# Kernel tuning notes

Measured on AMD Instinct MI355X. Metric: run time of the kernel, lower is better.

The kernel has to match this reference:

```python
import jax, jax.numpy as jnp
import numpy as np
from jax import lax

B, L, H = 2, 1024, 1024
D = 2048          # intermediate_size
N = 16            # ssm state size
K = 4             # conv kernel
R = 64            # time_step_rank


def setup_inputs() -> dict:
    key = jax.random.key(0)
    ks = jax.random.split(key, 10)
    def nrm(k, shape, scale=0.02):
        return jax.random.normal(k, shape, dtype=jnp.float32) * scale
    A = jnp.arange(1, N + 1, dtype=jnp.float32)[None, :] * jnp.ones((D, 1), jnp.float32)
    return {
        "hidden_states": jax.random.normal(ks[0], (B, L, H), dtype=jnp.float32),
        "W_in":  nrm(ks[1], (2 * D, H)),
        "conv_w": nrm(ks[2], (D, 1, K), 0.1),
        "conv_b": nrm(ks[3], (D,), 0.1),
        "W_x":   nrm(ks[4], (R + 2 * N, D)),
        "W_dt":  nrm(ks[5], (D, R), 0.1),
        "b_dt":  jnp.full((D,), -4.6, jnp.float32),  # softplus(-4.6) ~ 0.01 dt init
        "A_log": jnp.log(A),
        "D_param": jnp.ones((D,), jnp.float32),
        "W_out": nrm(ks[6], (H, D)),
    }


def _mamba_forward(hidden_states, W_in, conv_w, conv_b, W_x, W_dt, b_dt, A_log, D_param, W_out):
    silu = jax.nn.silu
    # in_proj -> [B, L, 2D], chunk into x and gate
    proj = jnp.einsum("blh,eh->ble", hidden_states, W_in)
    x, gate = jnp.split(proj, 2, axis=-1)           # [B,L,D] each
    # depthwise causal conv over time: [B,D,L]
    xc = x.swapaxes(1, 2)
    xc = lax.conv_general_dilated(
        xc, conv_w, window_strides=(1,), padding=[(K - 1, 0)],
        dimension_numbers=("NCH", "OIH", "NCH"), feature_group_count=D)
    x = silu(xc + conv_b[None, :, None]).swapaxes(1, 2)   # [B,L,D]
    # x_proj -> dt, Bmat, Cmat
    ssm_p = jnp.einsum("bld,rd->blr", x, W_x)             # [B,L,R+2N]
    dt_lr, Bm, Cm = ssm_p[..., :R], ssm_p[..., R:R + N], ssm_p[..., R + N:]
    dt = jax.nn.softplus(jnp.einsum("blr,dr->bld", dt_lr, W_dt) + b_dt)  # [B,L,D]
    A = -jnp.exp(A_log)                                   # [D,N]
    dA = jnp.exp(dt[..., None] * A[None, None])           # [B,L,D,N]
    dBu = dt[..., None] * Bm[:, :, None, :] * x[..., None]  # [B,L,D,N]
    # selective scan over time
    def step(h, inp):
        dA_t, dBu_t, C_t = inp                            # [B,D,N],[B,D,N],[B,N]
        h = dA_t * h + dBu_t
        y = jnp.einsum("bdn,bn->bd", h, C_t)
        return h, y
    h0 = jnp.zeros((B, D, N), dt.dtype)
    _, ys = lax.scan(step, h0, (dA.swapaxes(0, 1), dBu.swapaxes(0, 1), Cm.swapaxes(0, 1)))
    y = ys.swapaxes(0, 1)                                 # [B,L,D]
    y = (y + x * D_param[None, None, :]) * silu(gate)
    return jnp.einsum("bld,hd->blh", y, W_out)            # [B,L,H]


def reference(hidden_states, W_in, conv_w, conv_b, W_x, W_dt, b_dt, A_log, D_param, W_out):
    return _mamba_forward(hidden_states, W_in, conv_w, conv_b, W_x, W_dt, b_dt, A_log, D_param, W_out)
```

## Files before the change

### kernel.cpp

```cpp
#include <hip/hip_runtime.h>
#include <hip/hip_bf16.h>
#include <math.h>

#define B_ 2
#define L_ 1024
#define H_ 1024
#define D_ 2048
#define N_ 16
#define R_ 64
#define NCK 32
#define CL 32

typedef short short8 __attribute__((ext_vector_type(8)));
typedef float floatx4 __attribute__((ext_vector_type(4)));

__device__ __forceinline__ float siluf(float g) {
    return g / (1.0f + __expf(-g));
}

__device__ __forceinline__ unsigned short f2bf(float f) {
    unsigned int u = __float_as_uint(f);
    u = (u + 0x7fffu + ((u >> 16) & 1u)) >> 16;
    return (unsigned short)u;
}

__device__ __forceinline__ float bf2f(unsigned short u) {
    return __uint_as_float(((unsigned int)u) << 16);
}

__device__ __forceinline__ void gl2lds(const unsigned short* g, unsigned short* l) {
    __builtin_amdgcn_global_load_lds(
        (const __attribute__((address_space(1))) unsigned int*)g,
        (__attribute__((address_space(3))) unsigned int*)l, 16, 0, 0);
}

#define Q0 524288
#define Q1 1572864
#define Q2 2097152
#define Q3 2146304
#define Q4 2179072
__global__ __launch_bounds__(256) void cvt_all(
    const float* __restrict__ i0, const float* __restrict__ i1,
    const float* __restrict__ i2, const float* __restrict__ i3,
    const float* __restrict__ i4,
    unsigned short* __restrict__ o0, unsigned short* __restrict__ o1,
    unsigned short* __restrict__ o2, unsigned short* __restrict__ o3,
    unsigned short* __restrict__ o4)
{
    int q = blockIdx.x * 256 + threadIdx.x;
    if (q >= Q4) return;
    const float* in; unsigned short* out; int base;
    if (q < Q0)      { in = i0; out = o0; base = 0; }
    else if (q < Q1) { in = i1; out = o1; base = Q0; }
    else if (q < Q2) { in = i2; out = o2; base = Q1; }
    else if (q < Q3) { in = i3; out = o3; base = Q2; }
    else             { in = i4; out = o4; base = Q3; }
    int i = (q - base) * 4;
    float4 v = *(const float4*)(in + i);
    ushort4 o;
    o.x = f2bf(v.x); o.y = f2bf(v.y); o.z = f2bf(v.z); o.w = f2bf(v.w);
    *(ushort4*)(out + i) = o;
}

template<int EPI>
__global__ __launch_bounds__(256) void gemm_bf16_nt(
    const unsigned short* __restrict__ A, const unsigned short* __restrict__ Bm,
    float* __restrict__ C, int K, int Ncols, int ldc, int kChunk, int nMax,
    size_t partStride, float* __restrict__ C2)
{
    __shared__ unsigned short As[128 * 32];
    __shared__ unsigned short Bs[128 * 32];
    const int tid  = threadIdx.x;
    const int lane = tid & 63;
    const int wave = tid >> 6;
    const int wm = (wave >> 1) * 64;
    const int wn = (wave & 1) * 64;
    const int lr   = lane & 15;
    const int quad = lane >> 4;
    const int m0 = blockIdx.y * 128;
    const int n0 = blockIdx.x * 128;
    const int k0 = blockIdx.z * kChunk;

    const int srow = wave * 32 + (lane >> 2);
    const int sq   = (lane & 3) * 8;
    unsigned short* AsB0 = &As[(wave * 32) * 32];
    unsigned short* AsB1 = &As[(wave * 32 + 16) * 32];
    unsigned short* BsB0 = &Bs[(wave * 32) * 32];
    unsigned short* BsB1 = &Bs[(wave * 32 + 16) * 32];
    const size_t aoff0 = (size_t)(m0 + srow) * K + sq;
    const size_t aoff1 = (size_t)(m0 + srow + 16) * K + sq;
    const size_t boff0 = (size_t)min(n0 + srow, nMax - 1) * K + sq;
    const size_t boff1 = (size_t)min(n0 + srow + 16, nMax - 1) * K + sq;

    floatx4 acc[4][4];
#pragma unroll
    for (int mi = 0; mi < 4; ++mi)
#pragma unroll
        for (int ni = 0; ni < 4; ++ni)
            acc[mi][ni] = (floatx4){0.f, 0.f, 0.f, 0.f};

    for (int kt = k0; kt < k0 + kChunk; kt += 32) {
        __syncthreads();
        gl2lds(A + aoff0 + kt, AsB0);
        gl2lds(A + aoff1 + kt, AsB1);
        gl2lds(Bm + boff0 + kt, BsB0);
        gl2lds(Bm + boff1 + kt, BsB1);
        __syncthreads();
        short8 af[4], bf[4];
#pragma unroll
        for (int mi = 0; mi < 4; ++mi)
            af[mi] = *(const short8*)&As[(wm + mi * 16 + lr) * 32 + quad * 8];
#pragma unroll
        for (int ni = 0; ni < 4; ++ni)
            bf[ni] = *(const short8*)&Bs[(wn + ni * 16 + lr) * 32 + quad * 8];
#pragma unroll
        for (int mi = 0; mi < 4; ++mi)
#pragma unroll
            for (int ni = 0; ni < 4; ++ni)
                acc[mi][ni] = __builtin_amdgcn_mfma_f32_16x16x32_bf16(
                    af[mi], bf[ni], acc[mi][ni], 0, 0, 0);
    }

    float* Cz = C + (size_t)blockIdx.z * partStride;
#pragma unroll
    for (int mi = 0; mi < 4; ++mi)
#pragma unroll
        for (int ni = 0; ni < 4; ++ni) {
            const int rr = m0 + wm + mi * 16 + quad * 4;
            const int cc = n0 + wn + ni * 16 + lr;
            if (cc >= Ncols) continue;
            if (EPI == 4) {
                if (n0 < 2048) {
                    float4 v = make_float4(acc[mi][ni][0], acc[mi][ni][1],
                                           acc[mi][ni][2], acc[mi][ni][3]);
                    *(float4*)&C[(size_t)cc * ldc + rr] = v;
                } else {
#pragma unroll
                    for (int r = 0; r < 4; ++r)
                        C2[(size_t)(rr + r) * 2048 + (cc - 2048)] = acc[mi][ni][r];
                }
            } else {
#pragma unroll
                for (int r = 0; r < 4; ++r)
                    Cz[(size_t)(rr + r) * ldc + cc] = acc[mi][ni][r];
            }
        }
}

__global__ __launch_bounds__(256) void reduce_ssm(
    const float* __restrict__ P, float* __restrict__ ssm_p,
    unsigned short* __restrict__ sp64)
{
    const int q = blockIdx.x * 256 + threadIdx.x;
    const int m = q / 24;
    const int c = (q - m * 24) * 4;
    const size_t idx = (size_t)m * 96 + c;
    float4 s = make_float4(0.f, 0.f, 0.f, 0.f);
#pragma unroll
    for (int z = 0; z < 16; ++z) {
        float4 v = *(const float4*)(P + (size_t)z * (2048 * 96) + idx);
        s.x += v.x; s.y += v.y; s.z += v.z; s.w += v.w;
    }
    *(float4*)(ssm_p + idx) = s;
    if (c < 64) {
        ushort4 o;
        o.x = f2bf(s.x); o.y = f2bf(s.y); o.z = f2bf(s.z); o.w = f2bf(s.w);
        *(ushort4*)(sp64 + (size_t)m * 64 + c) = o;
    }
}

__global__ __launch_bounds__(256) void reduce_out(
    const float* __restrict__ P, float* __restrict__ out)
{
    const size_t i = ((size_t)blockIdx.x * 256 + threadIdx.x) * 4;
    float4 a = *(const float4*)(P + i);
    float4 b = *(const float4*)(P + 2097152 + i);
    float4 c = *(const float4*)(P + 2 * 2097152 + i);
    float4 d = *(const float4*)(P + 3 * 2097152 + i);
    *(float4*)(out + i) = make_float4(a.x + b.x + c.x + d.x,
                                      a.y + b.y + c.y + d.y,
                                      a.z + b.z + c.z + d.z,
                                      a.w + b.w + c.w + d.w);
}

__global__ __launch_bounds__(256) void dt_gemm(
    const unsigned short* __restrict__ A,
    const unsigned short* __restrict__ Bm,
    float* __restrict__ C,
    const float* __restrict__ bias)
{
    __shared__ unsigned short As[64 * 72];
    __shared__ unsigned short Bs[64 * 72];
    const int tid = threadIdx.x;
    const int lane = tid & 63;
    const int wave = tid >> 6;
    const int lr = lane & 15;
    const int quad = lane >> 4;
    const int n0 = blockIdx.x * 64;
    const int m0 = blockIdx.y * 64;

    {
        const int row = tid >> 3;
        const int cq = (tid & 7) * 8;
        uint4 a0 = *(const uint4*)(A + (size_t)(m0 + row) * 64 + cq);
        uint4 a1 = *(const uint4*)(A + (size_t)(m0 + 32 + row) * 64 + cq);
        uint4 b0 = *(const uint4*)(Bm + (size_t)(n0 + row) * 64 + cq);
        uint4 b1 = *(const uint4*)(Bm + (size_t)(n0 + 32 + row) * 64 + cq);
        *(uint4*)&As[row * 72 + cq] = a0;
        *(uint4*)&As[(32 + row) * 72 + cq] = a1;
        *(uint4*)&Bs[row * 72 + cq] = b0;
        *(uint4*)&Bs[(32 + row) * 72 + cq] = b1;
    }
    __syncthreads();

    floatx4 acc[4];
#pragma unroll
    for (int ni = 0; ni < 4; ++ni) acc[ni] = (floatx4){0.f, 0.f, 0.f, 0.f};

#pragma unroll
    for (int kt = 0; kt < 64; kt += 32) {
        short8 af = *(const short8*)&As[(wave * 16 + lr) * 72 + kt + quad * 8];
#pragma unroll
        for (int ni = 0; ni < 4; ++ni) {
            short8 bf = *(const short8*)&Bs[(ni * 16 + lr) * 72 + kt + quad * 8];
            acc[ni] = __builtin_amdgcn_mfma_f32_16x16x32_bf16(af, bf, acc[ni], 0, 0, 0);
        }
    }

    const int rr = m0 + wave * 16 + quad * 4;
#pragma unroll
    for (int ni = 0; ni < 4; ++ni) {
        const int cc = n0 + ni * 16 + lr;
        const float bv = bias[cc];
#pragma unroll
        for (int r = 0; r < 4; ++r) {
            const float z = acc[ni][r] + bv;
            const float spv = fmaxf(z, 0.f) + __logf(1.f + __expf(-fabsf(z)));
            C[(size_t)(rr + r) * 2048 + cc] = spv;
        }
    }
}

__global__ __launch_bounds__(256) void conv_silu_kernel(
    const float* __restrict__ projx, const float* __restrict__ conv_w,
    const float* __restrict__ conv_b, unsigned short* __restrict__ x_bf)
{
    __shared__ unsigned short tile[64][72];
    const int t = threadIdx.x;
    const int d0 = blockIdx.x * 64;
    const int lt0 = blockIdx.y * 64;
    const int b = blockIdx.z;
    const int dl = t & 63;
    const int seg = t >> 6;
    const int d = d0 + dl;
    const int l0 = lt0 + seg * 16;
    const float* row = projx + (size_t)d * 2048 + b * 1024;
    const float w0 = conv_w[d * 4 + 0], w1 = conv_w[d * 4 + 1];
    const float w2 = conv_w[d * 4 + 2], w3 = conv_w[d * 4 + 3];
    const float bias = conv_b[d];

    float p[19];
    p[0] = (l0 >= 3) ? row[l0 - 3] : 0.f;
    p[1] = (l0 >= 2) ? row[l0 - 2] : 0.f;
    p[2] = (l0 >= 1) ? row[l0 - 1] : 0.f;
#pragma unroll
    for (int j = 0; j < 16; j += 4) {
        float4 q = *(const float4*)(row + l0 + j);
        p[3 + j] = q.x; p[4 + j] = q.y; p[5 + j] = q.z; p[6 + j] = q.w;
    }
#pragma unroll
    for (int j = 0; j < 16; ++j) {
        float v = siluf(bias + w0 * p[j] + w1 * p[j + 1] + w2 * p[j + 2] + w3 * p[j + 3]);
        tile[seg * 16 + j][dl] = f2bf(v);
    }
    __syncthreads();

    const int ml = t >> 2;
    const int c = t & 3;
    short8 s0 = *(const short8*)&tile[ml][c * 16];
    short8 s1 = *(const short8*)&tile[ml][c * 16 + 8];
    unsigned short* dst = x_bf + (size_t)(b * 1024 + lt0 + ml) * 2048 + d0 + c * 16;
    *(short8*)dst = s0;
    *(short8*)(dst + 8) = s1;
}

__global__ __launch_bounds__(256) void scan_p1(
    const float* __restrict__ dt, const unsigned short* __restrict__ x_bf,
    const float* __restrict__ sp, const float* __restrict__ A_log,
    float* __restrict__ Pch, float* __restrict__ Hch)
{
    __shared__ float sB[CL][16];
    const int tid = threadIdx.x;
    const int d = blockIdx.x * 256 + tid;
    const int ck = blockIdx.y;
    const int b = blockIdx.z;
    const int mb = b * 1024 + ck * CL;

    if (tid < CL * 4) {
        int row = tid >> 2, q = (tid & 3) * 4;
        *(float4*)&sB[row][q] = *(const float4*)(sp + (size_t)(mb + row) * 96 + 64 + q);
    }
    float An2[16];
    {
        const float* al = A_log + d * 16;
#pragma unroll
        for (int j = 0; j < 16; j += 4) {
            float4 a4 = *(const float4*)(al + j);
            An2[j + 0] = -__expf(a4.x) * 1.44269504f;
            An2[j + 1] = -__expf(a4.y) * 1.44269504f;
            An2[j + 2] = -__expf(a4.z) * 1.44269504f;
            An2[j + 3] = -__expf(a4.w) * 1.44269504f;
        }
    }
    __syncthreads();

    float h[16];
#pragma unroll
    for (int n = 0; n < 16; ++n) h[n] = 0.f;
    float dts = 0.f;

    for (int l = 0; l < CL; ++l) {
        const size_t off = (size_t)(mb + l) * 2048 + d;
        const float dtv = dt[off];
        const float xv = bf2f(x_bf[off]);
        const float u = dtv * xv;
        dts += dtv;
        float4 B0 = *(const float4*)&sB[l][0];
        float4 B1 = *(const float4*)&sB[l][4];
        float4 B2 = *(const float4*)&sB[l][8];
        float4 B3 = *(const float4*)&sB[l][12];
        float Bv[16] = {B0.x, B0.y, B0.z, B0.w, B1.x, B1.y, B1.z, B1.w,
                        B2.x, B2.y, B2.z, B2.w, B3.x, B3.y, B3.z, B3.w};
#pragma unroll
        for (int n = 0; n < 16; ++n) {
            const float dA = __builtin_amdgcn_exp2f(dtv * An2[n]);
            h[n] = fmaf(dA, h[n], Bv[n] * u);
        }
    }

    const size_t base = ((size_t)(b * NCK + ck) * 2048 + d) * 16;
#pragma unroll
    for (int j = 0; j < 16; j += 4) {
        float4 pv = make_float4(__builtin_amdgcn_exp2f(dts * An2[j]),
                                __builtin_amdgcn_exp2f(dts * An2[j + 1]),
                                __builtin_amdgcn_exp2f(dts * An2[j + 2]),
                                __builtin_amdgcn_exp2f(dts * An2[j + 3]));
        *(float4*)(Pch + base + j) = pv;
        *(float4*)(Hch + base + j) = make_float4(h[j], h[j + 1], h[j + 2], h[j + 3]);
    }
}

__global__ __launch_bounds__(256) void scan_combine(
    float* __restrict__ Pch, const float* __restrict__ Hch)
{
    const int flat = blockIdx.x * 256 + threadIdx.x;
    const int dn = flat & 32767;
    const int b = flat >> 15;
    float hin = 0.f;
#pragma unroll 4
    for (int ck = 0; ck < NCK; ++ck) {
        const size_t a = ((size_t)(b * NCK + ck) << 15) + dn;
        const float p = Pch[a];
        const float hc = Hch[a];
        Pch[a] = hin;
        hin = fmaf(p, hin, hc);
    }
}

__global__ __launch_bounds__(256) void scan_p2(
    const float* __restrict__ dt, const unsigned short* __restrict__ x_bf,
    const float* __restrict__ gate, const float* __restrict__ sp,
    const float* __restrict__ A_log, const float* __restrict__ Dp,
    const float* __restrict__ Hin, unsigned short* __restrict__ y_bf)
{
    __shared__ float sBC[CL][32];
    const int tid = threadIdx.x;
    const int d = blockIdx.x * 256 + tid;
    const int ck = blockIdx.y;
    const int b = blockIdx.z;
    const int mb = b * 1024 + ck * CL;

    {
        int row = tid >> 3, q = (tid & 7) * 4;
        *(float4*)&sBC[row][q] = *(const float4*)(sp + (size_t)(mb + row) * 96 + 64 + q);
    }
    float An2[16];
    {
        const float* al = A_log + d * 16;
#pragma unroll
        for (int j = 0; j < 16; j += 4) {
            float4 a4 = *(const float4*)(al + j);
            An2[j + 0] = -__expf(a4.x) * 1.44269504f;
            An2[j + 1] = -__expf(a4.y) * 1.44269504f;
            An2[j + 2] = -__expf(a4.z) * 1.44269504f;
            An2[j + 3] = -__expf(a4.w) * 1.44269504f;
        }
    }
    float h[16];
    {
        const size_t base = ((size_t)(b * NCK + ck) * 2048 + d) * 16;
#pragma unroll
        for (int j = 0; j < 16; j += 4) {
            float4 hv = *(const float4*)(Hin + base + j);
            h[j] = hv.x; h[j + 1] = hv.y; h[j + 2] = hv.z; h[j + 3] = hv.w;
        }
    }
    const float Dv = Dp[d];
    __syncthreads();

    for (int l = 0; l < CL; ++l) {
        const size_t off = (size_t)(mb + l) * 2048 + d;
        const float dtv = dt[off];
        const float xv = bf2f(x_bf[off]);
        const float gv = gate[off];
        const float u = dtv * xv;
        float4 B0 = *(const float4*)&sBC[l][0];
        float4 B1 = *(const float4*)&sBC[l][4];
        float4 B2 = *(const float4*)&sBC[l][8];
        float4 B3 = *(const float4*)&sBC[l][12];
        float Bv[16] = {B0.x, B0.y, B0.z, B0.w, B1.x, B1.y, B1.z, B1.w,
                        B2.x, B2.y, B2.z, B2.w, B3.x, B3.y, B3.z, B3.w};
#pragma unroll
        for (int n = 0; n < 16; ++n) {
            const float dA = __builtin_amdgcn_exp2f(dtv * An2[n]);
            h[n] = fmaf(dA, h[n], Bv[n] * u);
        }
        float4 C0 = *(const float4*)&sBC[l][16];
        float4 C1 = *(const float4*)&sBC[l][20];
        float4 C2 = *(const float4*)&sBC[l][24];
        float4 C3 = *(const float4*)&sBC[l][28];
        float Cv[16] = {C0.x, C0.y, C0.z, C0.w, C1.x, C1.y, C1.z, C1.w,
                        C2.x, C2.y, C2.z, C2.w, C3.x, C3.y, C3.z, C3.w};
        float p = 0.f;
#pragma unroll
        for (int n = 0; n < 16; ++n)
            p = fmaf(h[n], Cv[n], p);
        y_bf[off] = f2bf(fmaf(xv, Dv, p) * siluf(gv));
    }
}

extern "C" void kernel_launch(void* const* d_in, const int* in_sizes, int n_in,
                              void* d_out, int out_size, void* d_ws, size_t ws_size,
                              hipStream_t stream)
{
    const float* hs     = (const float*)d_in[0];
    const float* W_in   = (const float*)d_in[1];
    const float* conv_w = (const float*)d_in[2];
    const float* conv_b = (const float*)d_in[3];
    const float* W_x    = (const float*)d_in[4];
    const float* W_dt   = (const float*)d_in[5];
    const float* b_dt   = (const float*)d_in[6];
    const float* A_log  = (const float*)d_in[7];
    const float* Dp     = (const float*)d_in[8];
    const float* W_out  = (const float*)d_in[9];
    float* out = (float*)d_out;

    float* ws    = (float*)d_ws;
    float* gate  = ws;
    float* dtb   = gate + (size_t)4194304;
    float* projx = dtb + (size_t)4194304;
    float* ssm_p = projx + (size_t)4194304;
    unsigned short* hs_bf    = (unsigned short*)(ssm_p + 196608);
    unsigned short* W_in_bf  = hs_bf + (size_t)2097152;
    unsigned short* W_out_bf = W_in_bf + (size_t)4194304;
    unsigned short* W_x_bf   = W_out_bf + (size_t)2097152;
    unsigned short* W_dt_bf  = W_x_bf + (size_t)196608;
    unsigned short* sp64_bf  = W_dt_bf + (size_t)131072;
    unsigned short* x_bf     = sp64_bf + (size_t)131072;
    float* P1   = projx;
    float* Pch  = projx;
    float* Hch  = projx + (size_t)2097152;
    float* Pout = gate;
    unsigned short* y_bf = hs_bf;

    const int M = B_ * L_;

    cvt_all<<<(Q4 + 255) / 256, 256, 0, stream>>>(
        hs, W_in, W_out, W_x, W_dt, hs_bf, W_in_bf, W_out_bf, W_x_bf, W_dt_bf);

    gemm_bf16_nt<4><<<dim3(4096 / 128, M / 128, 1), 256, 0, stream>>>(
        hs_bf, W_in_bf, projx, 1024, 4096, 2048, 1024, 4096, 0, gate);

    conv_silu_kernel<<<dim3(D_ / 64, L_ / 64, B_), 256, 0, stream>>>(
        projx, conv_w, conv_b, x_bf);

    gemm_bf16_nt<0><<<dim3(1, M / 128, 16), 256, 0, stream>>>(
        x_bf, W_x_bf, P1, 2048, 96, 96, 128, 96, (size_t)2048 * 96, nullptr);

    reduce_ssm<<<(2048 * 24) / 256, 256, 0, stream>>>(P1, ssm_p, sp64_bf);

    dt_gemm<<<dim3(2048 / 64, 2048 / 64), 256, 0, stream>>>(
        sp64_bf, W_dt_bf, dtb, b_dt);

    scan_p1<<<dim3(D_ / 256, NCK, B_), 256, 0, stream>>>(
        dtb, x_bf, ssm_p, A_log, Pch, Hch);
    scan_combine<<<(B_ * D_ * 16) / 256, 256, 0, stream>>>(Pch, Hch);
    scan_p2<<<dim3(D_ / 256, NCK, B_), 256, 0, stream>>>(
        dtb, x_bf, gate, ssm_p, A_log, Dp, Pch, y_bf);

    gemm_bf16_nt<0><<<dim3(1024 / 128, M / 128, 4), 256, 0, stream>>>(
        y_bf, W_out_bf, Pout, 2048, 1024, 1024, 512, 1024, (size_t)2048 * 1024, nullptr);

    reduce_out<<<(2048 * 1024 / 4) / 256, 256, 0, stream>>>(Pout, out);
}
```

Baseline: 237.0 us.

## Store projected x and dt intermediates in bf16 with LDS-staged transposed epilogue

The in_proj GEMM now writes the transposed x half as bf16, staging the tile through shared memory so each row is written with coalesced 16-byte stores. The conv kernel reads this bf16 buffer, and dt_gemm writes softplus(dt) as bf16, which both scan passes then read. This halves the memory traffic for two large [B,L,D] intermediates. The cost is reduced precision on x before the conv and on dt, which feeds the exponentials in the scan, plus extra syncthreads in the GEMM epilogue.

```diff
diff --git a/kernel.cpp b/kernel.cpp
--- a/kernel.cpp
+++ b/kernel.cpp
@@ -121,30 +121,67 @@
                     af[mi], bf[ni], acc[mi][ni], 0, 0, 0);
     }
 
-    float* Cz = C + (size_t)blockIdx.z * partStride;
-#pragma unroll
-    for (int mi = 0; mi < 4; ++mi)
-#pragma unroll
-        for (int ni = 0; ni < 4; ++ni) {
-            const int rr = m0 + wm + mi * 16 + quad * 4;
-            const int cc = n0 + wn + ni * 16 + lr;
-            if (cc >= Ncols) continue;
-            if (EPI == 4) {
-                if (n0 < 2048) {
-                    float4 v = make_float4(acc[mi][ni][0], acc[mi][ni][1],
-                                           acc[mi][ni][2], acc[mi][ni][3]);
-                    *(float4*)&C[(size_t)cc * ldc + rr] = v;
-                } else {
+    if constexpr (EPI == 4) {
+        if (n0 < 2048) {
+            __shared__ unsigned short Ct[64 * 136];
+            unsigned short* Cb = (unsigned short*)C;
+#pragma unroll
+            for (int h = 0; h < 2; ++h) {
+                __syncthreads();
+                if ((wave & 1) == h) {
+#pragma unroll
+                    for (int mi = 0; mi < 4; ++mi)
+#pragma unroll
+                        for (int ni = 0; ni < 4; ++ni) {
+                            const int ccl = ni * 16 + lr;
+                            const int rrl = wm + mi * 16 + quad * 4;
+                            ushort4 v;
+                            v.x = f2bf(acc[mi][ni][0]);
+                            v.y = f2bf(acc[mi][ni][1]);
+                            v.z = f2bf(acc[mi][ni][2]);
+                            v.w = f2bf(acc[mi][ni][3]);
+                            *(ushort4*)&Ct[ccl * 136 + rrl] = v;
+                        }
+                }
+                __syncthreads();
+                const int row = tid >> 2;
+                const int mq = (tid & 3) * 32;
+                uint4 w0 = *(const uint4*)&Ct[row * 136 + mq];
+                uint4 w1 = *(const uint4*)&Ct[row * 136 + mq + 8];
+                uint4 w2 = *(const uint4*)&Ct[row * 136 + mq + 16];
+                uint4 w3 = *(const uint4*)&Ct[row * 136 + mq + 24];
+                unsigned short* dst = Cb + (size_t)(n0 + h * 64 + row) * 2048 + m0 + mq;
+                *(uint4*)dst = w0;
+                *(uint4*)(dst + 8) = w1;
+                *(uint4*)(dst + 16) = w2;
+                *(uint4*)(dst + 24) = w3;
+            }
+        } else {
+#pragma unroll
+            for (int mi = 0; mi < 4; ++mi)
+#pragma unroll
+                for (int ni = 0; ni < 4; ++ni) {
+                    const int rr = m0 + wm + mi * 16 + quad * 4;
+                    const int cc = n0 + wn + ni * 16 + lr - 2048;
 #pragma unroll
                     for (int r = 0; r < 4; ++r)
-                        C2[(size_t)(rr + r) * 2048 + (cc - 2048)] = acc[mi][ni][r];
+                        C2[(size_t)(rr + r) * 2048 + cc] = acc[mi][ni][r];
                 }
-            } else {
+        }
+    } else {
+        float* Cz = C + (size_t)blockIdx.z * partStride;
+#pragma unroll
+        for (int mi = 0; mi < 4; ++mi)
+#pragma unroll
+            for (int ni = 0; ni < 4; ++ni) {
+                const int rr = m0 + wm + mi * 16 + quad * 4;
+                const int cc = n0 + wn + ni * 16 + lr;
+                if (cc >= Ncols) continue;
 #pragma unroll
                 for (int r = 0; r < 4; ++r)
                     Cz[(size_t)(rr + r) * ldc + cc] = acc[mi][ni][r];
             }
-        }
+    }
 }
 
 __global__ __launch_bounds__(256) void reduce_ssm(
@@ -186,7 +223,7 @@
 __global__ __launch_bounds__(256) void dt_gemm(
     const unsigned short* __restrict__ A,
     const unsigned short* __restrict__ Bm,
-    float* __restrict__ C,
+    unsigned short* __restrict__ C,
     const float* __restrict__ bias)
 {
     __shared__ unsigned short As[64 * 72];
@@ -236,13 +273,13 @@
         for (int r = 0; r < 4; ++r) {
             const float z = acc[ni][r] + bv;
             const float spv = fmaxf(z, 0.f) + __logf(1.f + __expf(-fabsf(z)));
-            C[(size_t)(rr + r) * 2048 + cc] = spv;
+            C[(size_t)(rr + r) * 2048 + cc] = f2bf(spv);
         }
     }
 }
 
 __global__ __launch_bounds__(256) void conv_silu_kernel(
-    const float* __restrict__ projx, const float* __restrict__ conv_w,
+    const unsigned short* __restrict__ projx, const float* __restrict__ conv_w,
     const float* __restrict__ conv_b, unsigned short* __restrict__ x_bf)
 {
     __shared__ unsigned short tile[64][72];
@@ -254,19 +291,23 @@
     const int seg = t >> 6;
     const int d = d0 + dl;
     const int l0 = lt0 + seg * 16;
-    const float* row = projx + (size_t)d * 2048 + b * 1024;
+    const unsigned short* row = projx + (size_t)d * 2048 + b * 1024;
     const float w0 = conv_w[d * 4 + 0], w1 = conv_w[d * 4 + 1];
     const float w2 = conv_w[d * 4 + 2], w3 = conv_w[d * 4 + 3];
     const float bias = conv_b[d];
 
     float p[19];
-    p[0] = (l0 >= 3) ? row[l0 - 3] : 0.f;
-    p[1] = (l0 >= 2) ? row[l0 - 2] : 0.f;
-    p[2] = (l0 >= 1) ? row[l0 - 1] : 0.f;
-#pragma unroll
-    for (int j = 0; j < 16; j += 4) {
-        float4 q = *(const float4*)(row + l0 + j);
-        p[3 + j] = q.x; p[4 + j] = q.y; p[5 + j] = q.z; p[6 + j] = q.w;
+    p[0] = (l0 >= 3) ? bf2f(row[l0 - 3]) : 0.f;
+    p[1] = (l0 >= 2) ? bf2f(row[l0 - 2]) : 0.f;
+    p[2] = (l0 >= 1) ? bf2f(row[l0 - 1]) : 0.f;
+    {
+        short8 q0 = *(const short8*)(row + l0);
+        short8 q1 = *(const short8*)(row + l0 + 8);
+#pragma unroll
+        for (int j = 0; j < 8; ++j) {
+            p[3 + j] = bf2f((unsigned short)q0[j]);
+            p[11 + j] = bf2f((unsigned short)q1[j]);
+        }
     }
 #pragma unroll
     for (int j = 0; j < 16; ++j) {
@@ -285,7 +326,7 @@
 }
 
 __global__ __launch_bounds__(256) void scan_p1(
-    const float* __restrict__ dt, const unsigned short* __restrict__ x_bf,
+    const unsigned short* __restrict__ dt, const unsigned short* __restrict__ x_bf,
     const float* __restrict__ sp, const float* __restrict__ A_log,
     float* __restrict__ Pch, float* __restrict__ Hch)
 {
@@ -321,7 +362,7 @@
 
     for (int l = 0; l < CL; ++l) {
         const size_t off = (size_t)(mb + l) * 2048 + d;
-        const float dtv = dt[off];
+        const float dtv = bf2f(dt[off]);
         const float xv = bf2f(x_bf[off]);
         const float u = dtv * xv;
         dts += dtv;
@@ -368,7 +409,7 @@
 }
 
 __global__ __launch_bounds__(256) void scan_p2(
-    const float* __restrict__ dt, const unsigned short* __restrict__ x_bf,
+    const unsigned short* __restrict__ dt, const unsigned short* __restrict__ x_bf,
     const float* __restrict__ gate, const float* __restrict__ sp,
     const float* __restrict__ A_log, const float* __restrict__ Dp,
     const float* __restrict__ Hin, unsigned short* __restrict__ y_bf)
@@ -410,7 +451,7 @@
 
     for (int l = 0; l < CL; ++l) {
         const size_t off = (size_t)(mb + l) * 2048 + d;
-        const float dtv = dt[off];
+        const float dtv = bf2f(dt[off]);
         const float xv = bf2f(x_bf[off]);
         const float gv = gate[off];
         const float u = dtv * xv;
@@ -457,9 +498,9 @@
 
     float* ws    = (float*)d_ws;
     float* gate  = ws;
-    float* dtb   = gate + (size_t)4194304;
-    float* projx = dtb + (size_t)4194304;
-    float* ssm_p = projx + (size_t)4194304;
+    float* dtb_region = gate + (size_t)4194304;
+    float* projx_region = dtb_region + (size_t)4194304;
+    float* ssm_p = projx_region + (size_t)4194304;
     unsigned short* hs_bf    = (unsigned short*)(ssm_p + 196608);
     unsigned short* W_in_bf  = hs_bf + (size_t)2097152;
     unsigned short* W_out_bf = W_in_bf + (size_t)4194304;
@@ -467,9 +508,11 @@
     unsigned short* W_dt_bf  = W_x_bf + (size_t)196608;
     unsigned short* sp64_bf  = W_dt_bf + (size_t)131072;
     unsigned short* x_bf     = sp64_bf + (size_t)131072;
-    float* P1   = projx;
-    float* Pch  = projx;
-    float* Hch  = projx + (size_t)2097152;
+    unsigned short* projx_bf = (unsigned short*)projx_region;
+    unsigned short* dt_bf    = (unsigned short*)dtb_region;
+    float* P1   = projx_region;
+    float* Pch  = projx_region;
+    float* Hch  = projx_region + (size_t)2097152;
     float* Pout = gate;
     unsigned short* y_bf = hs_bf;
 
@@ -479,10 +522,10 @@
         hs, W_in, W_out, W_x, W_dt, hs_bf, W_in_bf, W_out_bf, W_x_bf, W_dt_bf);
 
     gemm_bf16_nt<4><<<dim3(4096 / 128, M / 128, 1), 256, 0, stream>>>(
-        hs_bf, W_in_bf, projx, 1024, 4096, 2048, 1024, 4096, 0, gate);
+        hs_bf, W_in_bf, (float*)projx_bf, 1024, 4096, 2048, 1024, 4096, 0, gate);
 
     conv_silu_kernel<<<dim3(D_ / 64, L_ / 64, B_), 256, 0, stream>>>(
-        projx, conv_w, conv_b, x_bf);
+        projx_bf, conv_w, conv_b, x_bf);
 
     gemm_bf16_nt<0><<<dim3(1, M / 128, 16), 256, 0, stream>>>(
         x_bf, W_x_bf, P1, 2048, 96, 96, 128, 96, (size_t)2048 * 96, nullptr);
@@ -490,13 +533,13 @@
     reduce_ssm<<<(2048 * 24) / 256, 256, 0, stream>>>(P1, ssm_p, sp64_bf);
 
     dt_gemm<<<dim3(2048 / 64, 2048 / 64), 256, 0, stream>>>(
-        sp64_bf, W_dt_bf, dtb, b_dt);
+        sp64_bf, W_dt_bf, dt_bf, b_dt);
 
     scan_p1<<<dim3(D_ / 256, NCK, B_), 256, 0, stream>>>(
-        dtb, x_bf, ssm_p, A_log, Pch, Hch);
+        dt_bf, x_bf, ssm_p, A_log, Pch, Hch);
     scan_combine<<<(B_ * D_ * 16) / 256, 256, 0, stream>>>(Pch, Hch);
     scan_p2<<<dim3(D_ / 256, NCK, B_), 256, 0, stream>>>(
-        dtb, x_bf, gate, ssm_p, A_log, Dp, Pch, y_bf);
+        dt_bf, x_bf, gate, ssm_p, A_log, Dp, Pch, y_bf);
 
     gemm_bf16_nt<0><<<dim3(1024 / 128, M / 128, 4), 256, 0, stream>>>(
         y_bf, W_out_bf, Pout, 2048, 1024, 1024, 512, 1024, (size_t)2048 * 1024, nullptr);
```

Result: no change. 239.2 us (+1.0%).
